# Performance work log

Measured on AMD Instinct MI355X. Metric: run time of the kernel, lower is better.

Reference implementation:

```python
import jax, jax.numpy as jnp
import numpy as np

N, E, L, F, M = 512, 2048, 16, 16, 8
HOPS = 2      # egonet radius (k_hop_subgraph num_hops)
H = 128       # WL hash buckets
N_ITER = 3    # WeisfeilerLehman(n_iter=3)
TAU = 0.1     # soft-relabeling temperature


def setup_inputs():
    key = jax.random.key(0)
    k0, k1, k2, k3, k4, k5 = jax.random.split(key, 6)
    labels = jax.random.randint(k0, (N,), 0, L)
    x = jax.nn.one_hot(labels, L, dtype=jnp.float32)
    edge_index = jax.random.randint(k1, (2, E), 0, N)
    # filter adjacencies, built exactly as in GKernel.__init__:
    # symmetric 0/1 with zero diagonal
    A = jax.random.uniform(k2, (F, M, M))
    A = ((A + jnp.swapaxes(A, -1, -2)) > 1.0).astype(jnp.float32)
    A = A * (1.0 - jnp.eye(M, dtype=jnp.float32))
    Xlab = jax.random.randint(k3, (F, M), 0, L)
    X = jax.nn.one_hot(Xlab, L, dtype=jnp.float32)
    # injective label -> bucket embedding (random distinct buckets)
    E0 = jax.nn.one_hot(jax.random.permutation(k4, H)[:L], H, dtype=jnp.float32)
    # random projection used to hash (own-label, neighbor-multiset) signatures
    Rproj = jax.random.normal(k5, (2 * H, H), dtype=jnp.float32)
    return {"x": x, "edge_index": edge_index, "P": A, "X": X, "E0": E0, "Rproj": Rproj}


def _wl_features(c0, nbr_sum, mask, Rproj):
    # soft Weisfeiler-Lehman subtree features: at each iteration the new
    # node label is a hash of (own label, neighbor-label multiset); the
    # graph feature is the concatenated per-iteration label histograms.
    c = c0 * mask[:, None]                       # [n, H]
    feats = [c.sum(0)]
    for _ in range(N_ITER):
        sig = jnp.concatenate([c, nbr_sum(c)], axis=-1)        # [n, 2H]
        c = jax.nn.softmax((sig @ Rproj) / TAU, axis=-1) * mask[:, None]
        feats.append(c.sum(0))
    return jnp.concatenate(feats)                # [(N_ITER+1)*H]


def _max_comp_mask(A):
    # largest connected component via min-label propagation (max_comp)
    comp = jnp.arange(M, dtype=jnp.float32)
    Ab = A > 0
    for _ in range(M):
        nbr_min = jnp.min(jnp.where(Ab, comp[None, :], 1e9), axis=1)
        comp = jnp.minimum(comp, nbr_min)
    ci = comp.astype(jnp.int32)
    counts = jax.ops.segment_sum(jnp.ones(M, jnp.float32), ci, num_segments=M)
    best = jnp.argmax(counts)
    return (ci == best).astype(jnp.float32)


def reference(x, edge_index, P, X, E0, Rproj):
    # symmetrize edges (egonets / WL kernels are undirected)
    src = jnp.concatenate([edge_index[0], edge_index[1]])
    dst = jnp.concatenate([edge_index[1], edge_index[0]])
    # --- k-hop egonet node masks (compute_egonets) : reach[i, j] = 1 iff
    # node j is within HOPS hops of root i ---
    reach = jnp.eye(N, dtype=jnp.float32)
    for _ in range(HOPS):
        agg = jax.ops.segment_sum(reach[:, src].T, dst, num_segments=N).T
        reach = jnp.clip(reach + agg, 0.0, 1.0)
    c0 = x @ E0                                  # initial bucket labels [N, H]

    def ego_feat(mask):
        emask = (mask[src] * mask[dst])[:, None]
        def nbr(c):
            return jax.ops.segment_sum(c[src] * emask, dst, num_segments=N)
        return _wl_features(c0, nbr, mask, Rproj)

    ego_feats = jax.vmap(ego_feat)(reach)        # [N, (N_ITER+1)*H]

    def filt_feat(Af, Xf):
        mask = _max_comp_mask(Af)
        Am = Af * mask[:, None] * mask[None, :]
        return _wl_features(Xf @ E0, lambda c: Am @ c, mask, Rproj)

    filt_feats = jax.vmap(filt_feat)(P, X)       # [F, (N_ITER+1)*H]

    # normalized WL kernel: k(g1,g2)/sqrt(k(g1,g1) k(g2,g2)); sim.T -> [N, F]
    sim = filt_feats @ ego_feats.T               # [F, N]
    nf = jnp.linalg.norm(filt_feats, axis=-1)
    ng = jnp.linalg.norm(ego_feats, axis=-1)
    sim = sim / (nf[:, None] * ng[None, :] + 1e-12)
    return sim.T
```

## Files before the change

### kernel.cpp

```cpp
#include <hip/hip_runtime.h>
#include <hip/hip_bf16.h>
#include <cstdint>
#include <cstddef>

#define NN 512
#define NE 2048
#define NDIR 4096
#define LL 16
#define FF 16
#define MM 8
#define HH 128
#define NIT 3
#define NFEAT 512
#define TCAP 40960
#define ECAP 4096
#define ROSTRIDE 513
#define PTILE 32
#define SIGW 264

using bf16x8 = __attribute__((ext_vector_type(8))) short;
using f32x4 = __attribute__((ext_vector_type(4))) float;
using u16x8 = __attribute__((ext_vector_type(8))) unsigned short;

__device__ __forceinline__ unsigned short f2bf(float x) {
    union { float f; unsigned u; } v; v.f = x;
    unsigned r = v.u + 0x7FFFu + ((v.u >> 16) & 1u);
    return (unsigned short)(r >> 16);
}
__device__ __forceinline__ float bf2f(unsigned short b) {
    union { unsigned u; float f; } v; v.u = ((unsigned)b) << 16; return v.f;
}

__global__ void k_reach_init(unsigned* __restrict__ B) {
    int idx = blockIdx.x * blockDim.x + threadIdx.x;
    if (idx >= NN * 16) return;
    int j = idx >> 4, w = idx & 15;
    B[idx] = (w == (j >> 5)) ? (1u << (j & 31)) : 0u;
}

__global__ void k_copy_u32(const unsigned* __restrict__ s, unsigned* __restrict__ d, int n) {
    int i = blockIdx.x * blockDim.x + threadIdx.x;
    if (i < n) d[i] = s[i];
}

__global__ void k_hop_or(const int* __restrict__ ei, const unsigned* __restrict__ Bold,
                         unsigned* __restrict__ Bnew) {
    int idx = blockIdx.x * blockDim.x + threadIdx.x;
    if (idx >= NDIR * 16) return;
    int e = idx >> 4, w = idx & 15;
    int s = ei[e];
    int d = (e < NE) ? ei[e + NE] : ei[e - NE];
    unsigned v = Bold[s * 16 + w];
    if (v) atomicOr(&Bnew[d * 16 + w], v);
}

__global__ void k_compact(const unsigned* __restrict__ B, int* __restrict__ cnt,
                          short* __restrict__ list16, short* __restrict__ pos16) {
    int i = blockIdx.x;
    int lane = threadIdx.x;
    int wi = i >> 5;
    unsigned bi = 1u << (i & 31);
    int base = 0;
    for (int j0 = 0; j0 < NN; j0 += 64) {
        int j = j0 + lane;
        bool has = (B[j * 16 + wi] & bi) != 0u;
        unsigned long long mask = __ballot(has);
        int pre = __popcll(mask & ((1ull << lane) - 1ull));
        short pos = -1;
        if (has) {
            pos = (short)(base + pre);
            list16[i * NN + pos] = (short)j;
        }
        pos16[i * NN + j] = pos;
        base += __popcll(mask);
    }
    if (lane == 0) cnt[i] = base;
}

__global__ void k_scan(const int* __restrict__ cnt, int* __restrict__ nodeOff) {
    __shared__ int s[NN];
    int t = threadIdx.x;
    s[t] = cnt[t];
    __syncthreads();
    for (int off = 1; off < NN; off <<= 1) {
        int v = (t >= off) ? s[t - off] : 0;
        __syncthreads();
        s[t] += v;
        __syncthreads();
    }
    nodeOff[t + 1] = s[t];
    if (t == 0) nodeOff[0] = 0;
}

__global__ void k_build_csr(const int* __restrict__ ei, const int* __restrict__ cnt,
                            const short* __restrict__ pos16, const short* __restrict__ list16,
                            const int* __restrict__ nodeOff, int* __restrict__ rowOff,
                            short* __restrict__ colIdx, int* __restrict__ rootOf,
                            short* __restrict__ nodeIdx) {
    __shared__ short pos_s[NN];
    __shared__ int indeg[NN + 1];
    int i = blockIdx.x;
    int t = threadIdx.x;
    int c = cnt[i];
    int pb = nodeOff[i];
    for (int j = t; j < NN; j += 128) pos_s[j] = pos16[i * NN + j];
    for (int u = t; u <= c; u += 128) indeg[u] = 0;
    for (int u = t; u < c; u += 128) {
        int p = pb + u;
        if (p < TCAP) {
            rootOf[p] = i;
            nodeIdx[p] = list16[i * NN + u];
        }
    }
    __syncthreads();
    for (int e = t; e < NDIR; e += 128) {
        int s = ei[e];
        int d = (e < NE) ? ei[e + NE] : ei[e - NE];
        int sc = pos_s[s], dc = pos_s[d];
        if (sc >= 0 && dc >= 0) atomicAdd(&indeg[dc], 1);
    }
    __syncthreads();
    if (t == 0) {
        int run = 0;
        int* ro = rowOff + i * ROSTRIDE;
        for (int u = 0; u < c; ++u) {
            int v = indeg[u];
            ro[u] = run;
            indeg[u] = run;
            run += v;
        }
        ro[c] = run;
    }
    __syncthreads();
    short* col = colIdx + (size_t)i * ECAP;
    for (int e = t; e < NDIR; e += 128) {
        int s = ei[e];
        int d = (e < NE) ? ei[e + NE] : ei[e - NE];
        int sc = pos_s[s], dc = pos_s[d];
        if (sc >= 0 && dc >= 0) {
            int slot = atomicAdd(&indeg[dc], 1);
            col[slot] = (short)sc;
        }
    }
}

__global__ void k_c0(const float* __restrict__ x, const float* __restrict__ E0,
                     float* __restrict__ c0_all) {
    int n = blockIdx.x, h = threadIdx.x;
    float s = 0.f;
    for (int l = 0; l < LL; ++l) s += x[n * LL + l] * E0[l * HH + h];
    c0_all[n * HH + h] = s;
}

__global__ void k_feats0(const int* __restrict__ cnt, const short* __restrict__ list16,
                         const float* __restrict__ c0_all, float* __restrict__ feats) {
    int i = blockIdx.x, h = threadIdx.x;
    int c = cnt[i];
    float s = 0.f;
    for (int u = 0; u < c; ++u) s += c0_all[(size_t)list16[i * NN + u] * HH + h];
    feats[i * NFEAT + h] = s;
}

__global__ void k_splitR(const float* __restrict__ R, unsigned short* __restrict__ RTh,
                         unsigned short* __restrict__ RTl) {
    int n = blockIdx.x;
    int k = threadIdx.x;
    float x = R[k * HH + n];
    unsigned short h = f2bf(x);
    RTh[n * 256 + k] = h;
    RTl[n * 256 + k] = f2bf(x - bf2f(h));
}

__global__ __launch_bounds__(256) void k_projsm(
    const int* __restrict__ nodeOff, const int* __restrict__ rootOf,
    const int* __restrict__ rowOff, const short* __restrict__ colIdx,
    const short* __restrict__ nidx, const float* __restrict__ srcC,
    const unsigned short* __restrict__ RTh, const unsigned short* __restrict__ RTl,
    float* __restrict__ cNext, float* __restrict__ feats, int it) {
    __shared__ __align__(16) unsigned short sigH[PTILE][SIGW];
    __shared__ __align__(16) unsigned short sigL[PTILE][SIGW];
    __shared__ int groots[PTILE];
    int T = nodeOff[NN];
    if (T > TCAP) T = TCAP;
    int p0 = blockIdx.x * PTILE;
    if (p0 >= T) return;
    int t = threadIdx.x;
    if (t < PTILE) groots[t] = (p0 + t < T) ? rootOf[p0 + t] : -1;
    {
        int gr = t & 31;
        int gc0 = (t >> 5) * 16;
        float own[16], ga[16];
#pragma unroll
        for (int j = 0; j < 16; ++j) { own[j] = 0.f; ga[j] = 0.f; }
        int p = p0 + gr;
        if (p < T) {
            int i = rootOf[p];
            int pb = nodeOff[i];
            int u = p - pb;
            int srowO = nidx ? (int)nidx[p] : p;
            const float* so = &srcC[(size_t)srowO * HH + gc0];
#pragma unroll
            for (int q4 = 0; q4 < 4; ++q4) {
                float4 v = *(const float4*)&so[q4 * 4];
                own[q4 * 4 + 0] = v.x; own[q4 * 4 + 1] = v.y;
                own[q4 * 4 + 2] = v.z; own[q4 * 4 + 3] = v.w;
            }
            const int* ro = rowOff + i * ROSTRIDE;
            int r0 = ro[u], r1 = ro[u + 1];
            const short* col = colIdx + (size_t)i * ECAP;
            for (int e = r0; e < r1; ++e) {
                int q = pb + col[e];
                int srow = nidx ? (int)nidx[q] : q;
                const float* src = &srcC[(size_t)srow * HH + gc0];
                float4 v0 = *(const float4*)&src[0];
                float4 v1 = *(const float4*)&src[4];
                float4 v2 = *(const float4*)&src[8];
                float4 v3 = *(const float4*)&src[12];
                ga[0] += v0.x;  ga[1] += v0.y;  ga[2] += v0.z;  ga[3] += v0.w;
                ga[4] += v1.x;  ga[5] += v1.y;  ga[6] += v1.z;  ga[7] += v1.w;
                ga[8] += v2.x;  ga[9] += v2.y;  ga[10] += v2.z; ga[11] += v2.w;
                ga[12] += v3.x; ga[13] += v3.y; ga[14] += v3.z; ga[15] += v3.w;
            }
        }
        u16x8 oh[2], ol[2], nh[2], nl[2];
#pragma unroll
        for (int hlf = 0; hlf < 2; ++hlf)
#pragma unroll
            for (int j = 0; j < 8; ++j) {
                float ov = own[hlf * 8 + j], nv = ga[hlf * 8 + j];
                unsigned short ohb = f2bf(ov), nhb = f2bf(nv);
                oh[hlf][j] = ohb; ol[hlf][j] = f2bf(ov - bf2f(ohb));
                nh[hlf][j] = nhb; nl[hlf][j] = f2bf(nv - bf2f(nhb));
            }
#pragma unroll
        for (int hlf = 0; hlf < 2; ++hlf) {
            *(u16x8*)&sigH[gr][gc0 + hlf * 8] = oh[hlf];
            *(u16x8*)&sigL[gr][gc0 + hlf * 8] = ol[hlf];
            *(u16x8*)&sigH[gr][128 + gc0 + hlf * 8] = nh[hlf];
            *(u16x8*)&sigL[gr][128 + gc0 + hlf * 8] = nl[hlf];
        }
    }
    __syncthreads();
    int w = t >> 6, l = t & 63;
    int lm = l & 15, lk = l >> 4;
    f32x4 acc[2][2];
#pragma unroll
    for (int m = 0; m < 2; ++m)
#pragma unroll
        for (int n = 0; n < 2; ++n)
#pragma unroll
            for (int r = 0; r < 4; ++r) acc[m][n][r] = 0.f;
#pragma unroll
    for (int ks = 0; ks < 8; ++ks) {
        int ko = ks * 32 + lk * 8;
        bf16x8 aH[2], aL[2], bH[2], bL[2];
#pragma unroll
        for (int m = 0; m < 2; ++m) {
            aH[m] = *(const bf16x8*)&sigH[m * 16 + lm][ko];
            aL[m] = *(const bf16x8*)&sigL[m * 16 + lm][ko];
        }
#pragma unroll
        for (int n = 0; n < 2; ++n) {
            size_t cb = (size_t)(w * 32 + n * 16 + lm) * 256 + ko;
            bH[n] = *(const bf16x8*)&RTh[cb];
            bL[n] = *(const bf16x8*)&RTl[cb];
        }
#pragma unroll
        for (int m = 0; m < 2; ++m)
#pragma unroll
            for (int n = 0; n < 2; ++n) {
                acc[m][n] = __builtin_amdgcn_mfma_f32_16x16x32_bf16(aH[m], bH[n], acc[m][n], 0, 0, 0);
                acc[m][n] = __builtin_amdgcn_mfma_f32_16x16x32_bf16(aH[m], bL[n], acc[m][n], 0, 0, 0);
                acc[m][n] = __builtin_amdgcn_mfma_f32_16x16x32_bf16(aL[m], bH[n], acc[m][n], 0, 0, 0);
            }
    }
    __syncthreads();
    float (*exS)[132] = (float(*)[132])&sigH[0][0];
#pragma unroll
    for (int m = 0; m < 2; ++m)
#pragma unroll
        for (int n = 0; n < 2; ++n)
#pragma unroll
            for (int r = 0; r < 4; ++r)
                exS[m * 16 + lk * 4 + r][w * 32 + n * 16 + lm] = acc[m][n][r] * 10.0f;
    __syncthreads();
    {
        int rt = t >> 3, cs = (t & 7) * 16;
        float v[16];
#pragma unroll
        for (int q4 = 0; q4 < 4; ++q4) {
            float4 x = *(const float4*)&exS[rt][cs + q4 * 4];
            v[q4 * 4 + 0] = x.x; v[q4 * 4 + 1] = x.y;
            v[q4 * 4 + 2] = x.z; v[q4 * 4 + 3] = x.w;
        }
        float m = v[0];
#pragma unroll
        for (int j = 1; j < 16; ++j) m = fmaxf(m, v[j]);
#pragma unroll
        for (int o = 1; o < 8; o <<= 1) m = fmaxf(m, __shfl_xor(m, o));
        float s = 0.f;
#pragma unroll
        for (int j = 0; j < 16; ++j) { v[j] = expf(v[j] - m); s += v[j]; }
#pragma unroll
        for (int o = 1; o < 8; o <<= 1) s += __shfl_xor(s, o);
        float inv = 1.f / s;
#pragma unroll
        for (int j = 0; j < 16; ++j) v[j] *= inv;
        int p = p0 + rt;
        if (cNext && p < T) {
#pragma unroll
            for (int q4 = 0; q4 < 4; ++q4)
                *(float4*)&cNext[(size_t)p * HH + cs + q4 * 4] =
                    make_float4(v[q4 * 4], v[q4 * 4 + 1], v[q4 * 4 + 2], v[q4 * 4 + 3]);
        }
#pragma unroll
        for (int q4 = 0; q4 < 4; ++q4)
            *(float4*)&exS[rt][cs + q4 * 4] =
                make_float4(v[q4 * 4], v[q4 * 4 + 1], v[q4 * 4 + 2], v[q4 * 4 + 3]);
    }
    __syncthreads();
    if (t < HH) {
        float* fb = feats + it * HH + t;
        float a = 0.f;
        int cur = -1;
        for (int q = 0; q < PTILE; ++q) {
            int r = groots[q];
            if (r < 0) break;
            float v = exS[q][t];
            if (r == cur) {
                a += v;
            } else {
                if (cur >= 0) atomicAdd(&fb[(size_t)cur * NFEAT], a);
                cur = r;
                a = v;
            }
        }
        if (cur >= 0) atomicAdd(&fb[(size_t)cur * NFEAT], a);
    }
}

__global__ __launch_bounds__(1024) void k_filter(
    const float* __restrict__ P, const float* __restrict__ X,
    const float* __restrict__ E0, const float* __restrict__ R,
    float* __restrict__ filt_feats, float* __restrict__ filt_norm) {
    __shared__ float A_s[64], Am[64], mask_s[8];
    __shared__ float c_s[MM][HH], nb_s[MM][HH];
    __shared__ float fl[NFEAT];
    __shared__ float redm[MM][2], reds[MM][2];
    __shared__ float rr[8];
    int f = blockIdx.x;
    int t = threadIdx.x;
    int v = t >> 7;
    int h = t & 127;
    int lane = t & 63;
    int wid = (t >> 6) & 1;
    if (t < 64) A_s[t] = P[f * 64 + t];
    __syncthreads();
    if (t == 0) {
        float comp[8];
        for (int u = 0; u < 8; ++u) comp[u] = (float)u;
        for (int itr = 0; itr < 8; ++itr) {
            float nm[8];
            for (int u = 0; u < 8; ++u) {
                float mn = 1e9f;
                for (int uu = 0; uu < 8; ++uu)
                    if (A_s[u * 8 + uu] > 0.f) mn = fminf(mn, comp[uu]);
                nm[u] = mn;
            }
            for (int u = 0; u < 8; ++u) comp[u] = fminf(comp[u], nm[u]);
        }
        int counts[8] = {0, 0, 0, 0, 0, 0, 0, 0};
        int ci[8];
        for (int u = 0; u < 8; ++u) {
            ci[u] = (int)comp[u];
            counts[ci[u]]++;
        }
        int best = 0;
        for (int cc = 1; cc < 8; ++cc)
            if (counts[cc] > counts[best]) best = cc;
        for (int u = 0; u < 8; ++u) mask_s[u] = (ci[u] == best) ? 1.f : 0.f;
    }
    __syncthreads();
    if (t < 64) Am[t] = A_s[t] * mask_s[t >> 3] * mask_s[t & 7];
    {
        float s = 0.f;
        for (int l = 0; l < LL; ++l) s += X[f * MM * LL + v * LL + l] * E0[l * HH + h];
        c_s[v][h] = s * mask_s[v];
    }
    __syncthreads();
    if (v == 0) {
        float s = 0.f;
#pragma unroll
        for (int u = 0; u < 8; ++u) s += c_s[u][h];
        fl[h] = s;
    }
    for (int it = 1; it <= NIT; ++it) {
        {
            float s = 0.f;
#pragma unroll
            for (int u = 0; u < 8; ++u) s += Am[v * 8 + u] * c_s[u][h];
            nb_s[v][h] = s;
        }
        __syncthreads();
        float a0 = 0.f, a1 = 0.f;
        const float* Rp = R + h;
#pragma unroll 4
        for (int k = 0; k < 128; k += 4) {
            float4 cv = *(const float4*)&c_s[v][k];
            float4 nv = *(const float4*)&nb_s[v][k];
            a0 = fmaf(cv.x, Rp[(k + 0) * HH], a0);
            a1 = fmaf(cv.y, Rp[(k + 1) * HH], a1);
            a0 = fmaf(cv.z, Rp[(k + 2) * HH], a0);
            a1 = fmaf(cv.w, Rp[(k + 3) * HH], a1);
            a0 = fmaf(nv.x, Rp[(128 + k + 0) * HH], a0);
            a1 = fmaf(nv.y, Rp[(128 + k + 1) * HH], a1);
            a0 = fmaf(nv.z, Rp[(128 + k + 2) * HH], a0);
            a1 = fmaf(nv.w, Rp[(128 + k + 3) * HH], a1);
        }
        float lg = (a0 + a1) / 0.1f;
        float m = lg;
        for (int o = 32; o; o >>= 1) m = fmaxf(m, __shfl_xor(m, o));
        if (lane == 0) redm[v][wid] = m;
        __syncthreads();
        m = fmaxf(redm[v][0], redm[v][1]);
        float e = expf(lg - m);
        float ss = e;
        for (int o = 32; o; o >>= 1) ss += __shfl_xor(ss, o);
        if (lane == 0) reds[v][wid] = ss;
        __syncthreads();
        ss = reds[v][0] + reds[v][1];
        float val = (e / ss) * mask_s[v];
        c_s[v][h] = val;
        __syncthreads();
        if (v == 0) {
            float s = 0.f;
#pragma unroll
            for (int u = 0; u < 8; ++u) s += c_s[u][h];
            fl[it * HH + h] = s;
        }
        __syncthreads();
    }
    if (t < 512) {
        float val = fl[t];
        filt_feats[f * NFEAT + t] = val;
        float sq = val * val;
        for (int o = 32; o; o >>= 1) sq += __shfl_xor(sq, o);
        if (lane == 0) rr[t >> 6] = sq;
    }
    __syncthreads();
    if (t == 0) {
        float s = 0.f;
#pragma unroll
        for (int u = 0; u < 8; ++u) s += rr[u];
        filt_norm[f] = sqrtf(s);
    }
}

__global__ void k_sim(const float* __restrict__ ego_feats, const float* __restrict__ filt_feats,
                      const float* __restrict__ filt_norm, float* __restrict__ out) {
    __shared__ float red[2];
    int i = blockIdx.x, h = threadIdx.x;
    int lane = h & 63, wid = h >> 6;
    float e0 = ego_feats[i * NFEAT + h];
    float e1 = ego_feats[i * NFEAT + 128 + h];
    float e2 = ego_feats[i * NFEAT + 256 + h];
    float e3 = ego_feats[i * NFEAT + 384 + h];
    float sq = e0 * e0 + e1 * e1 + e2 * e2 + e3 * e3;
    for (int o = 32; o; o >>= 1) sq += __shfl_xor(sq, o);
    if (lane == 0) red[wid] = sq;
    __syncthreads();
    float ng = sqrtf(red[0] + red[1]);
    for (int f = 0; f < FF; ++f) {
        float d = filt_feats[f * NFEAT + h] * e0 + filt_feats[f * NFEAT + 128 + h] * e1 +
                  filt_feats[f * NFEAT + 256 + h] * e2 + filt_feats[f * NFEAT + 384 + h] * e3;
        for (int o = 32; o; o >>= 1) d += __shfl_xor(d, o);
        __syncthreads();
        if (lane == 0) red[wid] = d;
        __syncthreads();
        if (h == 0) out[i * FF + f] = (red[0] + red[1]) / (filt_norm[f] * ng + 1e-12f);
    }
}

extern "C" void kernel_launch(void* const* d_in, const int* in_sizes, int n_in,
                              void* d_out, int out_size, void* d_ws, size_t ws_size,
                              hipStream_t stream) {
    const float* x = (const float*)d_in[0];
    const int* ei = (const int*)d_in[1];
    const float* P = (const float*)d_in[2];
    const float* X = (const float*)d_in[3];
    const float* E0 = (const float*)d_in[4];
    const float* R = (const float*)d_in[5];
    float* out = (float*)d_out;

    char* w = (char*)d_ws;
    auto alloc = [&](size_t bytes) {
        char* p = w;
        w += (bytes + 255) & ~(size_t)255;
        return p;
    };
    unsigned* B0 = (unsigned*)alloc(NN * 16 * 4);
    unsigned* B1 = (unsigned*)alloc(NN * 16 * 4);
    int* cnt = (int*)alloc(NN * 4);
    int* nodeOff = (int*)alloc((NN + 1) * 4);
    int* rootOf = (int*)alloc(TCAP * 4);
    short* nodeIdx = (short*)alloc(TCAP * 2);
    short* list16 = (short*)alloc((size_t)NN * NN * 2);
    short* pos16 = (short*)alloc((size_t)NN * NN * 2);
    int* rowOff = (int*)alloc((size_t)NN * ROSTRIDE * 4);
    short* colIdx = (short*)alloc((size_t)NN * ECAP * 2);
    float* c0_all = (float*)alloc((size_t)NN * HH * 4);
    float* ego_feats = (float*)alloc((size_t)NN * NFEAT * 4);
    float* filt_feats = (float*)alloc((size_t)FF * NFEAT * 4);
    float* filt_norm = (float*)alloc(FF * 4);
    float* cA = (float*)alloc((size_t)TCAP * HH * 4);
    float* cB = (float*)alloc((size_t)TCAP * HH * 4);
    unsigned short* RTh = (unsigned short*)alloc(128 * 256 * 2);
    unsigned short* RTl = (unsigned short*)alloc(128 * 256 * 2);

    hipMemsetAsync(ego_feats, 0, (size_t)NN * NFEAT * 4, stream);

    k_reach_init<<<64, 128, 0, stream>>>(B0);
    k_copy_u32<<<64, 128, 0, stream>>>(B0, B1, NN * 16);
    k_hop_or<<<512, 128, 0, stream>>>(ei, B0, B1);
    k_copy_u32<<<64, 128, 0, stream>>>(B1, B0, NN * 16);
    k_hop_or<<<512, 128, 0, stream>>>(ei, B1, B0);
    k_compact<<<NN, 64, 0, stream>>>(B0, cnt, list16, pos16);
    k_scan<<<1, NN, 0, stream>>>(cnt, nodeOff);
    k_build_csr<<<NN, 128, 0, stream>>>(ei, cnt, pos16, list16, nodeOff, rowOff, colIdx,
                                        rootOf, nodeIdx);
    k_c0<<<NN, HH, 0, stream>>>(x, E0, c0_all);
    k_feats0<<<NN, HH, 0, stream>>>(cnt, list16, c0_all, ego_feats);
    k_splitR<<<128, 256, 0, stream>>>(R, RTh, RTl);

    const int NBLK = (TCAP + PTILE - 1) / PTILE;
    k_projsm<<<NBLK, 256, 0, stream>>>(nodeOff, rootOf, rowOff, colIdx, nodeIdx, c0_all,
                                       RTh, RTl, cB, ego_feats, 1);
    k_projsm<<<NBLK, 256, 0, stream>>>(nodeOff, rootOf, rowOff, colIdx, (const short*)nullptr,
                                       cB, RTh, RTl, cA, ego_feats, 2);
    k_projsm<<<NBLK, 256, 0, stream>>>(nodeOff, rootOf, rowOff, colIdx, (const short*)nullptr,
                                       cA, RTh, RTl, (float*)nullptr, ego_feats, 3);

    k_filter<<<FF, 1024, 0, stream>>>(P, X, E0, R, filt_feats, filt_norm);
    k_sim<<<NN, HH, 0, stream>>>(ego_feats, filt_feats, filt_norm, out);
}
```

Baseline: 318.7 us.

## Prefetch B fragments, swizzle block order, remap gather threads in projection kernel

The projection/softmax kernel now double-buffers the global loads of the split-bf16 Rproj fragments, fetching the next K-slice while MFMAs run on the current one. Block indices are swizzled into 8 strided groups, the signature-gather thread mapping changes so each row's 8 threads are adjacent, and launch bounds request 4 waves per SIMD. The aim is to hide global load latency and improve coalescing and occupancy, at the cost of more registers for the prefetch buffers. The swizzle assumes the grid size is a multiple of 8; otherwise some tiles may be skipped.

```diff
diff --git a/kernel.cpp b/kernel.cpp
--- a/kernel.cpp
+++ b/kernel.cpp
@@ -171,7 +171,7 @@
     RTl[n * 256 + k] = f2bf(x - bf2f(h));
 }
 
-__global__ __launch_bounds__(256) void k_projsm(
+__global__ __launch_bounds__(256, 4) void k_projsm(
     const int* __restrict__ nodeOff, const int* __restrict__ rootOf,
     const int* __restrict__ rowOff, const short* __restrict__ colIdx,
     const short* __restrict__ nidx, const float* __restrict__ srcC,
@@ -182,13 +182,15 @@
     __shared__ int groots[PTILE];
     int T = nodeOff[NN];
     if (T > TCAP) T = TCAP;
-    int p0 = blockIdx.x * PTILE;
+    int cpx = gridDim.x >> 3;
+    int swz = (blockIdx.x & 7) * cpx + (blockIdx.x >> 3);
+    int p0 = swz * PTILE;
     if (p0 >= T) return;
     int t = threadIdx.x;
     if (t < PTILE) groots[t] = (p0 + t < T) ? rootOf[p0 + t] : -1;
     {
-        int gr = t & 31;
-        int gc0 = (t >> 5) * 16;
+        int gr = t >> 3;
+        int gc0 = (t & 7) * 16;
         float own[16], ga[16];
 #pragma unroll
         for (int j = 0; j < 16; ++j) { own[j] = 0.f; ga[j] = 0.f; }
@@ -243,6 +245,10 @@
     __syncthreads();
     int w = t >> 6, l = t & 63;
     int lm = l & 15, lk = l >> 4;
+    const unsigned short* bH0p = RTh + (size_t)(w * 32 + lm) * 256 + lk * 8;
+    const unsigned short* bH1p = RTh + (size_t)(w * 32 + 16 + lm) * 256 + lk * 8;
+    const unsigned short* bL0p = RTl + (size_t)(w * 32 + lm) * 256 + lk * 8;
+    const unsigned short* bL1p = RTl + (size_t)(w * 32 + 16 + lm) * 256 + lk * 8;
     f32x4 acc[2][2];
 #pragma unroll
     for (int m = 0; m < 2; ++m)
@@ -250,28 +256,35 @@
         for (int n = 0; n < 2; ++n)
 #pragma unroll
             for (int r = 0; r < 4; ++r) acc[m][n][r] = 0.f;
+    bf16x8 pbH[2][2], pbL[2][2];
+    pbH[0][0] = *(const bf16x8*)bH0p;
+    pbH[0][1] = *(const bf16x8*)bH1p;
+    pbL[0][0] = *(const bf16x8*)bL0p;
+    pbL[0][1] = *(const bf16x8*)bL1p;
 #pragma unroll
     for (int ks = 0; ks < 8; ++ks) {
+        int cur = ks & 1, nxt = cur ^ 1;
+        if (ks < 7) {
+            int o = (ks + 1) * 32;
+            pbH[nxt][0] = *(const bf16x8*)(bH0p + o);
+            pbH[nxt][1] = *(const bf16x8*)(bH1p + o);
+            pbL[nxt][0] = *(const bf16x8*)(bL0p + o);
+            pbL[nxt][1] = *(const bf16x8*)(bL1p + o);
+        }
         int ko = ks * 32 + lk * 8;
-        bf16x8 aH[2], aL[2], bH[2], bL[2];
+        bf16x8 aH[2], aL[2];
 #pragma unroll
         for (int m = 0; m < 2; ++m) {
             aH[m] = *(const bf16x8*)&sigH[m * 16 + lm][ko];
             aL[m] = *(const bf16x8*)&sigL[m * 16 + lm][ko];
         }
 #pragma unroll
-        for (int n = 0; n < 2; ++n) {
-            size_t cb = (size_t)(w * 32 + n * 16 + lm) * 256 + ko;
-            bH[n] = *(const bf16x8*)&RTh[cb];
-            bL[n] = *(const bf16x8*)&RTl[cb];
-        }
-#pragma unroll
         for (int m = 0; m < 2; ++m)
 #pragma unroll
             for (int n = 0; n < 2; ++n) {
-                acc[m][n] = __builtin_amdgcn_mfma_f32_16x16x32_bf16(aH[m], bH[n], acc[m][n], 0, 0, 0);
-                acc[m][n] = __builtin_amdgcn_mfma_f32_16x16x32_bf16(aH[m], bL[n], acc[m][n], 0, 0, 0);
-                acc[m][n] = __builtin_amdgcn_mfma_f32_16x16x32_bf16(aL[m], bH[n], acc[m][n], 0, 0, 0);
+                acc[m][n] = __builtin_amdgcn_mfma_f32_16x16x32_bf16(aH[m], pbH[cur][n], acc[m][n], 0, 0, 0);
+                acc[m][n] = __builtin_amdgcn_mfma_f32_16x16x32_bf16(aH[m], pbL[cur][n], acc[m][n], 0, 0, 0);
+                acc[m][n] = __builtin_amdgcn_mfma_f32_16x16x32_bf16(aL[m], pbH[cur][n], acc[m][n], 0, 0, 0);
             }
     }
     __syncthreads();
```

After: 319.2 us. No clear change (+0.2%).
